# Optimization experiments

Hardware: AMD Instinct MI355X
Metric: run time of the kernel (lower is better)

## Reference

```python
import jax, jax.numpy as jnp
import numpy as np

B, N = 4, 8192


def _nn_idx(a, b):
    # For each point in a [B,Na,3], index of nearest point in b [B,Nb,3].
    # ||a-b||^2 = ||a||^2 - 2 a.b + ||b||^2 ; ||a||^2 is constant per row -> drop it.
    d = jnp.sum(b * b, axis=-1)[:, None, :] - 2.0 * jnp.einsum('bnd,bmd->bnm', a, b)
    return jnp.argmin(d, axis=-1)  # [B, Na]


def _thickness(white, pial):
    # Mirrors compute_thickness_vector: white = inner, pial = outer.
    bix = jnp.arange(white.shape[0])[:, None]
    i1 = _nn_idx(white, pial)            # NN in pial for each white point
    inner_th = pial[bix, i1] - white     # [B, Nw, 3]
    i2 = _nn_idx(pial, white)            # NN in white for each pial point
    outer_th = pial - white[bix, i2]     # [B, Np, 3]
    return inner_th, outer_th


def _msn(a, b):
    # MeanSquaredNormLoss with w=None: mean over all points of sum((a-b)^2, -1)
    return jnp.mean(jnp.sum((a - b) ** 2, axis=-1))


def _sym(a, b, i_a, i_b):
    # SymmetricMeanSquaredNormLoss.forward (batch_size > 1 path, no weights)
    bix = jnp.arange(a.shape[0])[:, None]
    return 0.5 * (_msn(a, b[bix, i_a]) + _msn(a[bix, i_b], b))


def setup_inputs() -> dict:
    key = jax.random.key(0)
    ks = jax.random.split(key, 8)
    return {
        'pred_white': jax.random.normal(ks[0], (B, N, 3), jnp.float32),
        'pred_pial': jax.random.normal(ks[1], (B, N, 3), jnp.float32),
        'true_white': jax.random.normal(ks[2], (B, N, 3), jnp.float32),
        'true_pial': jax.random.normal(ks[3], (B, N, 3), jnp.float32),
        'i_pred_white': jax.random.randint(ks[4], (B, N), 0, N, jnp.int32),
        'i_true_white': jax.random.randint(ks[5], (B, N), 0, N, jnp.int32),
        'i_pred_pial': jax.random.randint(ks[6], (B, N), 0, N, jnp.int32),
        'i_true_pial': jax.random.randint(ks[7], (B, N), 0, N, jnp.int32),
    }


def reference(pred_white, pred_pial, true_white, true_pial,
              i_pred_white, i_true_white, i_pred_pial, i_true_pial):
    yp_inner, yp_outer = _thickness(pred_white, pred_pial)
    yt_inner, yt_outer = _thickness(true_white, true_pial)
    return (0.5 * _sym(yp_inner, yt_inner, i_pred_white, i_true_white)
            + 0.5 * _sym(yp_outer, yt_outer, i_pred_pial, i_true_pial))
```

## Files before the change

### kernel.cpp

```cpp
#include <hip/hip_runtime.h>
#include <math.h>

#define BATCH 4
#define NPTS 8192
#define BN (BATCH * NPTS)
#define NZB 16
#define QK 8
#define QBLK (256 * QK)
#define SUBT 64


__device__ __forceinline__ void pick_ab(int z, const float* pw, const float* pp,
                                        const float* tw, const float* tp,
                                        const float** qa, const float** cb) {
  if (z == 0)      { *qa = pw; *cb = pp; }
  else if (z == 1) { *qa = pp; *cb = pw; }
  else if (z == 2) { *qa = tw; *cb = tp; }
  else             { *qa = tp; *cb = tw; }
}

template <int SPL>
__global__ __launch_bounds__(256, 4) void nn_partial_kernel(
    const float* __restrict__ pw, const float* __restrict__ pp,
    const float* __restrict__ tw, const float* __restrict__ tp,
    float* __restrict__ part_d, unsigned char* __restrict__ part_t) {
  constexpr int SLICE = NPTS / SPL;
  constexpr int NSUB = SLICE / SUBT;
  __shared__ float4 sh[SLICE];

  const int zb = blockIdx.z;
  const int z = zb >> 2;
  const int b = zb & 3;
  const float* qa;
  const float* cb;
  pick_ab(z, pw, pp, tw, tp, &qa, &cb);

  const int tid = threadIdx.x;
  const int cslice = blockIdx.y * SLICE;
  const float* cbb = cb + (size_t)b * NPTS * 3;

  for (int m = tid; m < SLICE; m += 256) {
    const float* c = cbb + (size_t)(cslice + m) * 3;
    const float bx = c[0], by = c[1], bz = c[2];
    sh[m] = make_float4(bx, by, bz, fmaf(bx, bx, fmaf(by, by, bz * bz)));
  }
  __syncthreads();

  const int qbase = blockIdx.x * QBLK;
  float qx[QK], qy[QK], qz[QK], dmin[QK];
  int tile[QK];
  #pragma unroll
  for (int k = 0; k < QK; ++k) {
    const int n = qbase + tid + k * 256;
    const float* q = qa + ((size_t)b * NPTS + n) * 3;
    qx[k] = -2.0f * q[0];
    qy[k] = -2.0f * q[1];
    qz[k] = -2.0f * q[2];
    dmin[k] = INFINITY;
    tile[k] = 0;
  }

  for (int sub = 0; sub < NSUB; ++sub) {
    float pre[QK];
    #pragma unroll
    for (int k = 0; k < QK; ++k) pre[k] = dmin[k];

    const int cb0 = sub * SUBT;
    #pragma unroll 2
    for (int p = 0; p < SUBT / 2; ++p) {
      const float4 c0 = sh[cb0 + 2 * p];
      const float4 c1 = sh[cb0 + 2 * p + 1];
      float t0[QK], t1[QK];
      #pragma unroll
      for (int k = 0; k < QK; ++k)
        t0[k] = fmaf(qx[k], c0.x, fmaf(qy[k], c0.y, fmaf(qz[k], c0.z, c0.w)));
      #pragma unroll
      for (int k = 0; k < QK; ++k)
        t1[k] = fmaf(qx[k], c1.x, fmaf(qy[k], c1.y, fmaf(qz[k], c1.z, c1.w)));
      #pragma unroll
      for (int k = 0; k < QK; ++k)
        dmin[k] = fminf(fminf(t0[k], t1[k]), dmin[k]);
    }
    const int g = blockIdx.y * NSUB + sub;
    #pragma unroll
    for (int k = 0; k < QK; ++k)
      tile[k] = (dmin[k] < pre[k]) ? g : tile[k];
  }

  #pragma unroll
  for (int k = 0; k < QK; ++k) {
    const int n = qbase + tid + k * 256;
    const size_t o = (size_t)blockIdx.y * (NZB * NPTS) + (size_t)zb * NPTS + n;
    part_d[o] = dmin[k];
    part_t[o] = (unsigned char)tile[k];
  }
}

template <int SPL>
__global__ __launch_bounds__(1024) void nn_merge_rescan_kernel(
    const float* __restrict__ pw, const float* __restrict__ pp,
    const float* __restrict__ tw, const float* __restrict__ tp,
    const float* __restrict__ part_d, const unsigned char* __restrict__ part_t,
    int* __restrict__ idx_all, double* __restrict__ acc,
    unsigned int* __restrict__ ticket) {
  __shared__ float md[16][64];
  __shared__ int mg[16][64];
  __shared__ float sdq[64];
  __shared__ int sgq[64];

  if (blockIdx.x == 0 && threadIdx.x == 0) { *acc = 0.0; *ticket = 0u; }

  const int tid = threadIdx.x;
  const int wv = tid >> 6;
  const int lane = tid & 63;
  const int qid0 = blockIdx.x * 64;

  {
    float bd = INFINITY;
    int bg = 0x7fffffff;
    for (int s = wv; s < SPL; s += 16) {
      const size_t o = (size_t)s * (NZB * NPTS) + qid0 + lane;
      const float d = part_d[o];
      const int g = part_t[o];
      if (d < bd || (d == bd && g < bg)) { bd = d; bg = g; }
    }
    md[wv][lane] = bd;
    mg[wv][lane] = bg;
  }
  __syncthreads();
  if (wv == 0) {
    float bd = md[0][lane];
    int bg = mg[0][lane];
    #pragma unroll
    for (int v = 1; v < 16; ++v) {
      const float d = md[v][lane];
      const int g = mg[v][lane];
      if (d < bd || (d == bd && g < bg)) { bd = d; bg = g; }
    }
    sdq[lane] = bd;
    sgq[lane] = bg;
  }
  __syncthreads();

  const int zb = qid0 >> 13;
  const int z = zb >> 2;
  const int b = zb & 3;
  const float* qa;
  const float* cb;
  pick_ab(z, pw, pp, tw, tp, &qa, &cb);
  const float* qb0 = qa + (size_t)b * NPTS * 3;
  const float* cbb = cb + (size_t)b * NPTS * 3;
  const int n0 = qid0 & (NPTS - 1);

  #pragma unroll
  for (int j = 0; j < 4; ++j) {
    const int lq = wv * 4 + j;
    const float best_d = sdq[lq];
    const int best_g = sgq[lq];
    const float* q = qb0 + (size_t)(n0 + lq) * 3;
    const float qx = -2.0f * q[0];
    const float qy = -2.0f * q[1];
    const float qz = -2.0f * q[2];
    const int m = best_g * SUBT + lane;
    const float* c = cbb + (size_t)m * 3;
    const float bx = c[0], by = c[1], bz = c[2];
    const float b2 = fmaf(bx, bx, fmaf(by, by, bz * bz));
    const float dd = fmaf(qx, bx, fmaf(qy, by, fmaf(qz, bz, b2)));
    const unsigned long long hit = __ballot(dd == best_d);
    if (lane == 0)
      idx_all[qid0 + lq] = best_g * SUBT + (__ffsll((long long)hit) - 1);
  }
}

__device__ __forceinline__ float3 ld3(const float* __restrict__ p, int i) {
  const float* q = p + (size_t)i * 3;
  return make_float3(q[0], q[1], q[2]);
}

__device__ __forceinline__ float diff_nrm2(float3 a1, float3 a2, float3 b1, float3 b2) {
  const float x = (a1.x - a2.x) - (b1.x - b2.x);
  const float y = (a1.y - a2.y) - (b1.y - b2.y);
  const float z = (a1.z - a2.z) - (b1.z - b2.z);
  return fmaf(x, x, fmaf(y, y, z * z));
}

__global__ __launch_bounds__(256) void loss_final_kernel(
    const float* __restrict__ pw, const float* __restrict__ pp,
    const float* __restrict__ tw, const float* __restrict__ tp,
    const int* __restrict__ ipw, const int* __restrict__ itw,
    const int* __restrict__ ipp, const int* __restrict__ itp,
    const int* __restrict__ idx_all, double* __restrict__ acc,
    unsigned int* __restrict__ ticket, float* __restrict__ out) {
  __shared__ double sd[4];

  const int gid = blockIdx.x * 256 + threadIdx.x;
  const int term = blockIdx.y;
  const int b = gid >> 13;
  const int n = gid & (NPTS - 1);
  const int base = b * NPTS;

  const float* PW = pw + (size_t)base * 3;
  const float* PP = pp + (size_t)base * 3;
  const float* TW = tw + (size_t)base * 3;
  const float* TP = tp + (size_t)base * 3;
  const int* I1P = idx_all + (0 * BATCH + b) * NPTS;
  const int* I2P = idx_all + (1 * BATCH + b) * NPTS;
  const int* I1T = idx_all + (2 * BATCH + b) * NPTS;
  const int* I2T = idx_all + (3 * BATCH + b) * NPTS;

  float sv;
  if (term == 0) {
    const int j = ipw[base + n];
    sv = diff_nrm2(ld3(PP, I1P[n]), ld3(PW, n), ld3(TP, I1T[j]), ld3(TW, j));
  } else if (term == 1) {
    const int k = itw[base + n];
    sv = diff_nrm2(ld3(PP, I1P[k]), ld3(PW, k), ld3(TP, I1T[n]), ld3(TW, n));
  } else if (term == 2) {
    const int j = ipp[base + n];
    sv = diff_nrm2(ld3(PP, n), ld3(PW, I2P[n]), ld3(TP, j), ld3(TW, I2T[j]));
  } else {
    const int k = itp[base + n];
    sv = diff_nrm2(ld3(PP, k), ld3(PW, I2P[k]), ld3(TP, n), ld3(TW, I2T[n]));
  }

  double ds = (double)sv;
  #pragma unroll
  for (int o = 32; o > 0; o >>= 1) ds += __shfl_down(ds, o, 64);
  if ((threadIdx.x & 63) == 0) sd[threadIdx.x >> 6] = ds;
  __syncthreads();

  if (threadIdx.x == 0) {
    const double bsum = sd[0] + sd[1] + sd[2] + sd[3];
    const double old = atomicAdd(acc, bsum);
    const unsigned int inc = 1u + (unsigned int)(((unsigned long long)
                             __double_as_longlong(old)) & 0ull);
    const unsigned int total = gridDim.x * gridDim.y;
    const unsigned int t = atomicAdd(ticket, inc);
    if (t == total - 1u) {
      const double fin = atomicAdd(acc, 0.0);
      out[0] = (float)(0.25 * fin / (double)BN);
    }
  }
}

template <int SPL>
static void run_pipeline(const float* pw, const float* pp, const float* tw,
                         const float* tp, const int* ipw, const int* itw,
                         const int* ipp, const int* itp, char* ws, float* out,
                         hipStream_t stream) {
  double* acc = (double*)ws;
  unsigned int* ticket = (unsigned int*)(ws + 8);
  int* idx_all = (int*)(ws + 64);
  float* part_d = (float*)(ws + 64 + (size_t)NZB * NPTS * 4);
  unsigned char* part_t =
      (unsigned char*)(ws + 64 + (size_t)NZB * NPTS * 4 +
                       (size_t)SPL * NZB * NPTS * 4);

  dim3 grid_nn(NPTS / QBLK, SPL, NZB);
  nn_partial_kernel<SPL><<<grid_nn, 256, 0, stream>>>(pw, pp, tw, tp, part_d,
                                                      part_t);
  nn_merge_rescan_kernel<SPL><<<(NZB * NPTS) / 64, 1024, 0, stream>>>(
      pw, pp, tw, tp, part_d, part_t, idx_all, acc, ticket);

  dim3 grid_loss(BN / 256, 4);
  loss_final_kernel<<<grid_loss, 256, 0, stream>>>(
      pw, pp, tw, tp, ipw, itw, ipp, itp, idx_all, acc, ticket, out);
}

extern "C" void kernel_launch(void* const* d_in, const int* in_sizes, int n_in,
                              void* d_out, int out_size, void* d_ws, size_t ws_size,
                              hipStream_t stream) {
  const float* pw = (const float*)d_in[0];
  const float* pp = (const float*)d_in[1];
  const float* tw = (const float*)d_in[2];
  const float* tp = (const float*)d_in[3];
  const int* ipw = (const int*)d_in[4];
  const int* itw = (const int*)d_in[5];
  const int* ipp = (const int*)d_in[6];
  const int* itp = (const int*)d_in[7];
  char* ws = (char*)d_ws;
  float* out = (float*)d_out;

  const size_t base_need = 64 + (size_t)NZB * NPTS * 4;
  const size_t per_spl = (size_t)NZB * NPTS * 5;
  if (ws_size >= base_need + 32 * per_spl) {
    run_pipeline<32>(pw, pp, tw, tp, ipw, itw, ipp, itp, ws, out, stream);
  } else if (ws_size >= base_need + 16 * per_spl) {
    run_pipeline<16>(pw, pp, tw, tp, ipw, itw, ipp, itp, ws, out, stream);
  } else {
    run_pipeline<8>(pw, pp, tw, tp, ipw, itw, ipp, itp, ws, out, stream);
  }
}
```

Measured before the change: 180.4 us.

## Compute NN distances with bf16x3 split MFMA and flagged exact rescan

Replaces the scalar FMA distance scan with MFMA 16x16x32 bf16 matrix ops. Candidate and query coordinates are split into hi/lo bf16 pairs so the product approximates fp32, and a pack kernel writes the candidate fragments to workspace first. The merge kernel flags every slice whose approximate minimum lies within a tolerance of the best and rescans those slices exactly in fp32 to recover the argmin. The risks are a missed true nearest neighbour if the bf16 error exceeds TAU, and extra rescan work when many slices fall within the tolerance.

```diff
diff --git a/kernel.cpp b/kernel.cpp
--- a/kernel.cpp
+++ b/kernel.cpp
@@ -5,10 +5,12 @@
 #define NPTS 8192
 #define BN (BATCH * NPTS)
 #define NZB 16
-#define QK 8
-#define QBLK (256 * QK)
-#define SUBT 64
-
+#define QN (NZB * NPTS)
+#define TAU 1.0e-2f
+
+
+using frag_ab = __attribute__((ext_vector_type(8))) short;
+using frag_cd = __attribute__((ext_vector_type(4))) float;
 
 __device__ __forceinline__ void pick_ab(int z, const float* pw, const float* pp,
                                         const float* tw, const float* tp,
@@ -19,14 +21,58 @@
   else             { *qa = tp; *cb = tw; }
 }
 
-template <int SPL>
-__global__ __launch_bounds__(256, 4) void nn_partial_kernel(
+__device__ __forceinline__ unsigned short f2bf(float x) {
+  unsigned int u = __float_as_uint(x);
+  u += 0x7fffu + ((u >> 16) & 1u);
+  return (unsigned short)(u >> 16);
+}
+__device__ __forceinline__ float bf2f(unsigned short h) {
+  return __uint_as_float(((unsigned int)h) << 16);
+}
+
+__global__ __launch_bounds__(256) void pack_kernel(
     const float* __restrict__ pw, const float* __restrict__ pp,
     const float* __restrict__ tw, const float* __restrict__ tp,
-    float* __restrict__ part_d, unsigned char* __restrict__ part_t) {
+    unsigned short* __restrict__ bpack) {
+  const int g = blockIdx.x * 256 + threadIdx.x;
+  const int zb = g >> 13;
+  const int n = g & (NPTS - 1);
+  const int z = zb >> 2;
+  const int b = zb & 3;
+  const float* qa;
+  const float* cb;
+  pick_ab(z, pw, pp, tw, tp, &qa, &cb);
+
+  const float* c = cb + ((size_t)b * NPTS + n) * 3;
+  const float bx = c[0], by = c[1], bz = c[2];
+  unsigned short bh[3], bl[3];
+  const float bf[3] = {bx, by, bz};
+  #pragma unroll
+  for (int d = 0; d < 3; ++d) {
+    bh[d] = f2bf(bf[d]);
+    bl[d] = f2bf(bf[d] - bf2f(bh[d]));
+  }
+  const float b2 = fmaf(bx, bx, fmaf(by, by, bz * bz));
+  const unsigned short b2h = f2bf(b2);
+  const unsigned short b2l = f2bf(b2 - bf2f(b2h));
+
+  unsigned short v[16] = {bh[0], bh[1], bh[2], bh[0], bh[1], bh[2],
+                          bl[0], bl[1], bl[2], bl[0], bl[1], bl[2],
+                          b2h, b2l, 0, 0};
+  uint4* dst = (uint4*)(bpack + (size_t)g * 16);
+  const uint4* src = (const uint4*)v;
+  dst[0] = src[0];
+  dst[1] = src[1];
+}
+
+template <int SPL>
+__global__ __launch_bounds__(256, 4) void nn_mfma_scan(
+    const float* __restrict__ pw, const float* __restrict__ pp,
+    const float* __restrict__ tw, const float* __restrict__ tp,
+    const unsigned short* __restrict__ bpack, float* __restrict__ part_d) {
   constexpr int SLICE = NPTS / SPL;
-  constexpr int NSUB = SLICE / SUBT;
-  __shared__ float4 sh[SLICE];
+  constexpr int NCT = SLICE / 16;
+  __shared__ unsigned short lds_b[SLICE * 16];
 
   const int zb = blockIdx.z;
   const int z = zb >> 2;
@@ -34,79 +80,104 @@
   const float* qa;
   const float* cb;
   pick_ab(z, pw, pp, tw, tp, &qa, &cb);
+  (void)cb;
 
   const int tid = threadIdx.x;
-  const int cslice = blockIdx.y * SLICE;
-  const float* cbb = cb + (size_t)b * NPTS * 3;
-
-  for (int m = tid; m < SLICE; m += 256) {
-    const float* c = cbb + (size_t)(cslice + m) * 3;
-    const float bx = c[0], by = c[1], bz = c[2];
-    sh[m] = make_float4(bx, by, bz, fmaf(bx, bx, fmaf(by, by, bz * bz)));
+
+  {
+    const uint4* src =
+        (const uint4*)(bpack + ((size_t)zb * NPTS + blockIdx.y * SLICE) * 16);
+    uint4* dst = (uint4*)lds_b;
+    for (int i = tid; i < SLICE * 2; i += 256) {
+      const int pg = i ^ ((i >> 3) & 6);
+      dst[pg] = src[i];
+    }
   }
   __syncthreads();
 
-  const int qbase = blockIdx.x * QBLK;
-  float qx[QK], qy[QK], qz[QK], dmin[QK];
-  int tile[QK];
-  #pragma unroll
-  for (int k = 0; k < QK; ++k) {
-    const int n = qbase + tid + k * 256;
+  const int wv = tid >> 6;
+  const int lane = tid & 63;
+  const int quad = lane >> 4;
+  const int col = lane & 15;
+  const int qbase = blockIdx.x * 256 + wv * 64;
+
+  frag_ab A[4];
+  #pragma unroll
+  for (int qt = 0; qt < 4; ++qt) {
+    const int n = qbase + qt * 16 + col;
     const float* q = qa + ((size_t)b * NPTS + n) * 3;
-    qx[k] = -2.0f * q[0];
-    qy[k] = -2.0f * q[1];
-    qz[k] = -2.0f * q[2];
-    dmin[k] = INFINITY;
-    tile[k] = 0;
-  }
-
-  for (int sub = 0; sub < NSUB; ++sub) {
-    float pre[QK];
-    #pragma unroll
-    for (int k = 0; k < QK; ++k) pre[k] = dmin[k];
-
-    const int cb0 = sub * SUBT;
-    #pragma unroll 2
-    for (int p = 0; p < SUBT / 2; ++p) {
-      const float4 c0 = sh[cb0 + 2 * p];
-      const float4 c1 = sh[cb0 + 2 * p + 1];
-      float t0[QK], t1[QK];
+    unsigned short h[3], l[3];
+    #pragma unroll
+    for (int d = 0; d < 3; ++d) {
+      const float a = q[d];
+      const unsigned short ah = f2bf(a);
+      const unsigned short al = f2bf(a - bf2f(ah));
+      h[d] = f2bf(-2.0f * bf2f(ah));
+      l[d] = f2bf(-2.0f * bf2f(al));
+    }
+    const short ONE = (short)0x3F80;
+    frag_ab q0, q1;
+    q0[0] = (short)h[0]; q0[1] = (short)h[1]; q0[2] = (short)h[2];
+    q0[3] = (short)l[0]; q0[4] = (short)l[1]; q0[5] = (short)l[2];
+    q0[6] = (short)h[0]; q0[7] = (short)h[1];
+    q1[0] = (short)h[2]; q1[1] = (short)l[0]; q1[2] = (short)l[1];
+    q1[3] = (short)l[2]; q1[4] = ONE;        q1[5] = ONE;
+    q1[6] = 0;           q1[7] = 0;
+    frag_ab az;
+    #pragma unroll
+    for (int j = 0; j < 8; ++j) az[j] = 0;
+    A[qt] = (quad == 0) ? q0 : (quad == 1) ? q1 : az;
+  }
+
+  float dmin[4][4];
+  #pragma unroll
+  for (int qt = 0; qt < 4; ++qt)
+    #pragma unroll
+    for (int r = 0; r < 4; ++r) dmin[qt][r] = INFINITY;
+
+  const frag_ab* lb = (const frag_ab*)lds_b;
+  const int half = quad & 1;
+
+  for (int ct = 0; ct < NCT; ++ct) {
+    const int g = (ct * 16 + col) * 2 + half;
+    const frag_ab Bf = lb[g ^ ((g >> 3) & 6)];
+    #pragma unroll
+    for (int qt = 0; qt < 4; ++qt) {
+      frag_cd cfr = {0.0f, 0.0f, 0.0f, 0.0f};
+      cfr = __builtin_amdgcn_mfma_f32_16x16x32_bf16(A[qt], Bf, cfr, 0, 0, 0);
       #pragma unroll
-      for (int k = 0; k < QK; ++k)
-        t0[k] = fmaf(qx[k], c0.x, fmaf(qy[k], c0.y, fmaf(qz[k], c0.z, c0.w)));
+      for (int r = 0; r < 4; ++r) dmin[qt][r] = fminf(dmin[qt][r], cfr[r]);
+    }
+  }
+
+  #pragma unroll
+  for (int off = 1; off < 16; off <<= 1)
+    #pragma unroll
+    for (int qt = 0; qt < 4; ++qt)
       #pragma unroll
-      for (int k = 0; k < QK; ++k)
-        t1[k] = fmaf(qx[k], c1.x, fmaf(qy[k], c1.y, fmaf(qz[k], c1.z, c1.w)));
+      for (int r = 0; r < 4; ++r)
+        dmin[qt][r] = fminf(dmin[qt][r], __shfl_xor(dmin[qt][r], off));
+
+  if (col == 0) {
+    #pragma unroll
+    for (int qt = 0; qt < 4; ++qt)
       #pragma unroll
-      for (int k = 0; k < QK; ++k)
-        dmin[k] = fminf(fminf(t0[k], t1[k]), dmin[k]);
-    }
-    const int g = blockIdx.y * NSUB + sub;
-    #pragma unroll
-    for (int k = 0; k < QK; ++k)
-      tile[k] = (dmin[k] < pre[k]) ? g : tile[k];
-  }
-
-  #pragma unroll
-  for (int k = 0; k < QK; ++k) {
-    const int n = qbase + tid + k * 256;
-    const size_t o = (size_t)blockIdx.y * (NZB * NPTS) + (size_t)zb * NPTS + n;
-    part_d[o] = dmin[k];
-    part_t[o] = (unsigned char)tile[k];
+      for (int r = 0; r < 4; ++r) {
+        const int m = qbase + qt * 16 + quad * 4 + r;
+        part_d[(size_t)blockIdx.y * QN + (size_t)zb * NPTS + m] = dmin[qt][r];
+      }
   }
 }
 
 template <int SPL>
-__global__ __launch_bounds__(1024) void nn_merge_rescan_kernel(
+__global__ __launch_bounds__(1024) void nn_merge_flag_rescan(
     const float* __restrict__ pw, const float* __restrict__ pp,
     const float* __restrict__ tw, const float* __restrict__ tp,
-    const float* __restrict__ part_d, const unsigned char* __restrict__ part_t,
-    int* __restrict__ idx_all, double* __restrict__ acc,
-    unsigned int* __restrict__ ticket) {
-  __shared__ float md[16][64];
-  __shared__ int mg[16][64];
-  __shared__ float sdq[64];
-  __shared__ int sgq[64];
+    const float* __restrict__ part_d, int* __restrict__ idx_all,
+    double* __restrict__ acc, unsigned int* __restrict__ ticket) {
+  constexpr int SLICE = NPTS / SPL;
+  constexpr int NIT = SLICE / 64;
+  __shared__ float sm[SPL][64];
 
   if (blockIdx.x == 0 && threadIdx.x == 0) { *acc = 0.0; *ticket = 0u; }
 
@@ -115,31 +186,8 @@
   const int lane = tid & 63;
   const int qid0 = blockIdx.x * 64;
 
-  {
-    float bd = INFINITY;
-    int bg = 0x7fffffff;
-    for (int s = wv; s < SPL; s += 16) {
-      const size_t o = (size_t)s * (NZB * NPTS) + qid0 + lane;
-      const float d = part_d[o];
-      const int g = part_t[o];
-      if (d < bd || (d == bd && g < bg)) { bd = d; bg = g; }
-    }
-    md[wv][lane] = bd;
-    mg[wv][lane] = bg;
-  }
-  __syncthreads();
-  if (wv == 0) {
-    float bd = md[0][lane];
-    int bg = mg[0][lane];
-    #pragma unroll
-    for (int v = 1; v < 16; ++v) {
-      const float d = md[v][lane];
-      const int g = mg[v][lane];
-      if (d < bd || (d == bd && g < bg)) { bd = d; bg = g; }
-    }
-    sdq[lane] = bd;
-    sgq[lane] = bg;
-  }
+  for (int s = wv; s < SPL; s += 16)
+    sm[s][lane] = part_d[(size_t)s * QN + qid0 + lane];
   __syncthreads();
 
   const int zb = qid0 >> 13;
@@ -155,20 +203,38 @@
   #pragma unroll
   for (int j = 0; j < 4; ++j) {
     const int lq = wv * 4 + j;
-    const float best_d = sdq[lq];
-    const int best_g = sgq[lq];
     const float* q = qb0 + (size_t)(n0 + lq) * 3;
     const float qx = -2.0f * q[0];
     const float qy = -2.0f * q[1];
     const float qz = -2.0f * q[2];
-    const int m = best_g * SUBT + lane;
-    const float* c = cbb + (size_t)m * 3;
-    const float bx = c[0], by = c[1], bz = c[2];
-    const float b2 = fmaf(bx, bx, fmaf(by, by, bz * bz));
-    const float dd = fmaf(qx, bx, fmaf(qy, by, fmaf(qz, bz, b2)));
-    const unsigned long long hit = __ballot(dd == best_d);
-    if (lane == 0)
-      idx_all[qid0 + lq] = best_g * SUBT + (__ffsll((long long)hit) - 1);
+
+    const float sv = (lane < SPL) ? sm[lane][lq] : INFINITY;
+    float mt = sv;
+    #pragma unroll
+    for (int off = 32; off > 0; off >>= 1) mt = fminf(mt, __shfl_xor(mt, off));
+    unsigned long long flags = __ballot(sv <= mt + TAU);
+
+    float bd = INFINITY;
+    int bi = 0x7fffffff;
+    while (flags) {
+      const int s = __ffsll((long long)flags) - 1;
+      flags &= flags - 1;
+      for (int it = 0; it < NIT; ++it) {
+        const int m = s * SLICE + it * 64 + lane;
+        const float* c = cbb + (size_t)m * 3;
+        const float bx = c[0], by = c[1], bz = c[2];
+        const float b2 = fmaf(bx, bx, fmaf(by, by, bz * bz));
+        const float dd = fmaf(qx, bx, fmaf(qy, by, fmaf(qz, bz, b2)));
+        if (dd < bd) { bd = dd; bi = m; }
+      }
+    }
+    #pragma unroll
+    for (int off = 32; off > 0; off >>= 1) {
+      const float od = __shfl_xor(bd, off);
+      const int oi = __shfl_xor(bi, off);
+      if (od < bd || (od == bd && oi < bi)) { bd = od; bi = oi; }
+    }
+    if (lane == 0) idx_all[qid0 + lq] = bi;
   }
 }
 
@@ -251,16 +317,17 @@
   double* acc = (double*)ws;
   unsigned int* ticket = (unsigned int*)(ws + 8);
   int* idx_all = (int*)(ws + 64);
-  float* part_d = (float*)(ws + 64 + (size_t)NZB * NPTS * 4);
-  unsigned char* part_t =
-      (unsigned char*)(ws + 64 + (size_t)NZB * NPTS * 4 +
-                       (size_t)SPL * NZB * NPTS * 4);
-
-  dim3 grid_nn(NPTS / QBLK, SPL, NZB);
-  nn_partial_kernel<SPL><<<grid_nn, 256, 0, stream>>>(pw, pp, tw, tp, part_d,
-                                                      part_t);
-  nn_merge_rescan_kernel<SPL><<<(NZB * NPTS) / 64, 1024, 0, stream>>>(
-      pw, pp, tw, tp, part_d, part_t, idx_all, acc, ticket);
+  float* part_d = (float*)(ws + 64 + (size_t)QN * 4);
+  unsigned short* bpack =
+      (unsigned short*)(ws + 64 + (size_t)QN * 4 + (size_t)SPL * QN * 4);
+
+  pack_kernel<<<QN / 256, 256, 0, stream>>>(pw, pp, tw, tp, bpack);
+
+  dim3 grid_scan(NPTS / 256, SPL, NZB);
+  nn_mfma_scan<SPL><<<grid_scan, 256, 0, stream>>>(pw, pp, tw, tp, bpack,
+                                                   part_d);
+  nn_merge_flag_rescan<SPL><<<QN / 64, 1024, 0, stream>>>(
+      pw, pp, tw, tp, part_d, idx_all, acc, ticket);
 
   dim3 grid_loss(BN / 256, 4);
   loss_final_kernel<<<grid_loss, 256, 0, stream>>>(
@@ -281,8 +348,8 @@
   char* ws = (char*)d_ws;
   float* out = (float*)d_out;
 
-  const size_t base_need = 64 + (size_t)NZB * NPTS * 4;
-  const size_t per_spl = (size_t)NZB * NPTS * 5;
+  const size_t base_need = 64 + (size_t)QN * 4 + (size_t)QN * 32;
+  const size_t per_spl = (size_t)QN * 4;
   if (ws_size >= base_need + 32 * per_spl) {
     run_pipeline<32>(pw, pp, tw, tp, ipw, itw, ipp, itp, ws, out, stream);
   } else if (ws_size >= base_need + 16 * per_spl) {
```

After: 221.1 us. 1.23x slower.
